# Kernel optimization log

Hardware: AMD Instinct MI355X
Metric: run time of the kernel (lower is better)

Reference implementation:

```python
import jax, jax.numpy as jnp
import numpy as np

EPS = 1e-7
B, C, IMG = 1024, 3, 32
NCLASS = 10
N_IN, L_IN, L_OUT = 64, 16, 16   # primary caps: 64 capsules of length 16; digit caps length 16
R_ITER = 3


def squash(c, axis):
    dot = jnp.sum(c * c, axis=axis, keepdims=True)
    return dot / (1.0 + dot) / jnp.sqrt(dot + EPS) * c


def conv2d(x, w, b, stride):
    y = jax.lax.conv_general_dilated(x, w, (stride, stride), 'VALID',
                                     dimension_numbers=('NCHW', 'OIHW', 'NCHW'))
    return y + b[None, :, None, None]


def setup_inputs() -> dict:
    key = jax.random.key(0)
    ks = jax.random.split(key, 16)
    inp = {
        'x': jax.random.uniform(ks[0], (B, C, IMG, IMG), dtype=jnp.float32),
        'y': jax.random.randint(ks[1], (B,), 0, NCLASS, dtype=jnp.int64),
        'conv1_w': 0.05 * jax.random.normal(ks[2], (128, C, 3, 3), jnp.float32),
        'conv1_b': jnp.zeros((128,), jnp.float32),
        'conv2_w': 0.05 * jax.random.normal(ks[3], (256, 128, 5, 5), jnp.float32),
        'conv2_b': jnp.zeros((256,), jnp.float32),
        'conv3_w': 0.05 * jax.random.normal(ks[4], (256, 256, 5, 5), jnp.float32),
        'conv3_b': jnp.zeros((256,), jnp.float32),
        'caps_w': 0.05 * jax.random.normal(ks[5], (N_IN, NCLASS, L_IN, L_OUT), jnp.float32),
        'caps_b': 0.05 * jax.random.normal(ks[6], (NCLASS, L_OUT), jnp.float32),
        'fc1_w': 0.05 * jax.random.normal(ks[7], (512, NCLASS * L_OUT), jnp.float32),
        'fc1_b': jnp.zeros((512,), jnp.float32),
        'fc2_w': 0.05 * jax.random.normal(ks[8], (1024, 512), jnp.float32),
        'fc2_b': jnp.zeros((1024,), jnp.float32),
        'fc3_w': 0.05 * jax.random.normal(ks[9], (IMG * IMG * C, 1024), jnp.float32),
        'fc3_b': jnp.zeros((IMG * IMG * C,), jnp.float32),
    }
    return inp


def reference(x, y, conv1_w, conv1_b, conv2_w, conv2_b, conv3_w, conv3_b,
              caps_w, caps_b, fc1_w, fc1_b, fc2_w, fc2_b, fc3_w, fc3_b):
    # CNN blocks
    h = jax.nn.relu(conv2d(x, conv1_w, conv1_b, 2))   # [B,128,15,15]
    h = jax.nn.relu(conv2d(h, conv2_w, conv2_b, 2))   # [B,256,6,6]
    h = jax.nn.relu(conv2d(h, conv3_w, conv3_b, 1))   # [B,256,2,2]

    # Primary capsules: [B,64,16], squashed along capsule-length axis
    prim = squash(h.reshape(h.shape[0], N_IN, L_IN), axis=-1)

    # u_hat[b,i,o,j] = sum_k W[i,o,k,j] * prim[b,i,k]  -> [B,64,10,16]
    u_hat = jnp.einsum('bik,iokj->bioj', prim, caps_w)
    u_hat_det = jax.lax.stop_gradient(u_hat)

    b_ij = jnp.zeros((h.shape[0], N_IN, NCLASS), dtype=u_hat.dtype)
    v = None
    for r in range(R_ITER):
        c_ij = jax.nn.softmax(b_ij, axis=2)           # over output capsules
        uh = u_hat if r == R_ITER - 1 else u_hat_det
        s = jnp.einsum('bio,bioj->boj', c_ij, uh) + caps_b   # [B,10,16]
        v = squash(s, axis=-1)
        if r < R_ITER - 1:
            agree = jnp.einsum('bioj,boj->bio', u_hat_det, jax.lax.stop_gradient(v))
            b_ij = b_ij + agree

    # capsule lengths: [B,10,1,1]
    v_lengths = jnp.sqrt(jnp.sum(v * v, axis=-1, keepdims=True) + EPS)[..., None]

    # reconstruction (mask by true label one-hot)
    one_hot = jax.nn.one_hot(y, NCLASS, dtype=v.dtype)       # [B,10]
    masked = (v * one_hot[:, :, None]).reshape(v.shape[0], NCLASS * L_OUT)
    h1 = jax.nn.relu(masked @ fc1_w.T + fc1_b)
    h2 = jax.nn.relu(h1 @ fc2_w.T + fc2_b)
    decoded = jax.nn.sigmoid(h2 @ fc3_w.T + fc3_b)           # [B,3072]
    return (v_lengths, decoded)
```

## Files before the change

### kernel.cpp

```cpp
#include <hip/hip_runtime.h>
#include <hip/hip_bf16.h>
#include <math.h>

#define EPSF 1e-7f

typedef __attribute__((ext_vector_type(8))) short bhalf8;
typedef __attribute__((ext_vector_type(4))) float floatx4;

__global__ __launch_bounds__(256) void conv1_kernel(
    const float* __restrict__ x, const float* __restrict__ w,
    const float* __restrict__ bias, __hip_bfloat16* __restrict__ out)
{
  __shared__ float wl[4096];
  __shared__ float bl[128];
  const int b0 = blockIdx.x * 2;
  const int t = threadIdx.x;
  for (int i = t; i < 4096; i += 256) {
    int oc = i >> 5, q = i & 31;
    wl[i] = (q < 27) ? w[oc*27 + q] : 0.f;
  }
  if (t < 128) bl[t] = bias[t];
  __syncthreads();
  if (t >= 225) return;
  const int py = t / 15, px = t % 15;
  float win[2][28];
  win[0][27] = 0.f; win[1][27] = 0.f;
#pragma unroll
  for (int im = 0; im < 2; ++im) {
    const float* xb = x + (size_t)(b0 + im) * 3072;
#pragma unroll
    for (int c = 0; c < 3; ++c)
#pragma unroll
      for (int ky = 0; ky < 3; ++ky)
#pragma unroll
        for (int kx = 0; kx < 3; ++kx)
          win[im][c*9 + ky*3 + kx] = xb[c*1024 + (py*2 + ky)*32 + (px*2 + kx)];
  }
#pragma unroll 1
  for (int oc0 = 0; oc0 < 128; oc0 += 32) {
    __hip_bfloat16 hv[2][32];
#pragma unroll
    for (int oc = 0; oc < 32; ++oc) {
      const float4* wp = (const float4*)&wl[(oc0 + oc) << 5];
      float a0 = bl[oc0 + oc], a1 = a0;
#pragma unroll
      for (int qq = 0; qq < 7; ++qq) {
        float4 wv = wp[qq];
        a0 = fmaf(win[0][qq*4+0], wv.x, a0); a1 = fmaf(win[1][qq*4+0], wv.x, a1);
        a0 = fmaf(win[0][qq*4+1], wv.y, a0); a1 = fmaf(win[1][qq*4+1], wv.y, a1);
        a0 = fmaf(win[0][qq*4+2], wv.z, a0); a1 = fmaf(win[1][qq*4+2], wv.z, a1);
        a0 = fmaf(win[0][qq*4+3], wv.w, a0); a1 = fmaf(win[1][qq*4+3], wv.w, a1);
      }
      hv[0][oc] = __float2bfloat16(fmaxf(a0, 0.f));
      hv[1][oc] = __float2bfloat16(fmaxf(a1, 0.f));
    }
#pragma unroll
    for (int qq = 0; qq < 4; ++qq) {
      int c16 = (oc0 >> 3) + qq;
#pragma unroll
      for (int im = 0; im < 2; ++im) {
        const uint4* src = (const uint4*)hv[im];
        *(uint4*)((char*)out + (size_t)(b0+im)*57600 + c16*3600 + t*16) = src[qq];
      }
    }
  }
}

__global__ __launch_bounds__(256) void prep_kernel(
    const float* __restrict__ conv2w, const float* __restrict__ conv3w,
    const float* __restrict__ capsw,  const float* __restrict__ fc1w,
    const float* __restrict__ fc2w,   const float* __restrict__ fc3w,
    __hip_bfloat16* __restrict__ wt2, __hip_bfloat16* __restrict__ wt3,
    __hip_bfloat16* __restrict__ cwt, float* __restrict__ fc1wt,
    __hip_bfloat16* __restrict__ wf2, __hip_bfloat16* __restrict__ wf3)
{
  const int t = threadIdx.x;
  int b = blockIdx.x;
  if (b < 12288) {
    int i = b*256 + t;
    wf3[i] = __float2bfloat16(fc3w[i]);
    return;
  }
  b -= 12288;
  if (b < 6400) {
    int i = b*256 + t;
    int s = i >> 14, r = i & 16383;
    int oc = r >> 6, kq = r & 63;
    int k = s*64 + kq;
    int tap = k >> 8, ic = k & 255;
    wt3[i] = __float2bfloat16(conv3w[(oc*256 + ic)*25 + tap]);
    return;
  }
  b -= 6400;
  if (b < 3200) {
    int i = b*256 + t;
    int s = i >> 13, r = i & 8191;
    int oc = r >> 5, kq = r & 31;
    int h = (s >= 50) ? 1 : 0;
    int r2 = s - h*50;
    int tap = r2 >> 1, q = r2 & 1;
    int ic = h*64 + q*32 + kq;
    wt2[i] = __float2bfloat16(conv2w[(oc*128 + ic)*25 + tap]);
    return;
  }
  b -= 3200;
  if (b < 2048) {
    int i = b*256 + t;
    wf2[i] = __float2bfloat16(fc2w[i]);
    return;
  }
  b -= 2048;
  if (b < 640) {
    int i2 = b*256 + t;
    int k = i2 & 15, j = (i2 >> 4) & 15, io = i2 >> 8;
    cwt[i2] = __float2bfloat16(capsw[(io*16 + k)*16 + j]);
    return;
  }
  b -= 640;
  {
    int i = b*256 + t;
    int j = i >> 9, n = i & 511;
    fc1wt[i] = fc1w[n*160 + j];
  }
}

__global__ __launch_bounds__(1024) void conv2_mfma_v2_kernel(
    const __hip_bfloat16* __restrict__ a,
    const __hip_bfloat16* __restrict__ wt,
    const float* __restrict__ bias,
    __hip_bfloat16* __restrict__ out,
    int img_base)
{
  __shared__ __align__(16) unsigned short Il[4*225*64];
  const int b0   = img_base + blockIdx.x * 4;
  const int t    = threadIdx.x;
  const int lane = t & 63;
  const int w    = t >> 6;
  const int wm   = w >> 3;
  const int wn   = w & 7;
  const int n    = lane & 15;
  const int g    = lane >> 4;

  const char* gB = (const char*)wt + (wn*32 + n)*64 + g*16;
  bhalf8 b00 = *(const bhalf8*)(gB);
  bhalf8 b01 = *(const bhalf8*)(gB + 1024);
  bhalf8 b10 = *(const bhalf8*)(gB + 16384);
  bhalf8 b11 = *(const bhalf8*)(gB + 16384 + 1024);

  int Abase[5], em[5];
#pragma unroll
  for (int mt = 0; mt < 5; ++mt) {
    int tile = wm*5 + mt;
    int m = tile*16 + n;
    if (m >= 144) m = 0;
    int img = m / 36, pos = m - img*36;
    int py = pos / 6, px = pos - py*6;
    int pixb = 30*py + 2*px;
    Abase[mt] = (img*225 + pixb) * 128;
    em[mt] = g + m;
  }

  floatx4 acc[5][2];
#pragma unroll
  for (int mt = 0; mt < 5; ++mt)
#pragma unroll
    for (int nt = 0; nt < 2; ++nt)
      acc[mt][nt] = (floatx4){0.f, 0.f, 0.f, 0.f};

  int s = 0;
#pragma unroll 1
  for (int h = 0; h < 2; ++h) {
    if (h) __syncthreads();
    for (int i = t; i < 7200; i += 1024) {
      int img = i / 1800;
      int r = i - img*1800;
      int p = r >> 3, c = r & 7;
      uint4 v = *(const uint4*)((const char*)a +
                (size_t)(b0+img)*57600 + (h*8 + c)*3600 + p*16);
      int px15 = p % 15, py15 = p / 15;
      int csw = (c + (px15 >> 1) + 6*(py15 >> 1) + ((img & 1) << 2)) & 7;
      *(uint4*)((char*)Il + (img*225 + p)*128 + csw*16) = v;
    }
    __syncthreads();

    int dpix = 0, kx = 0, ky = 0;
#pragma unroll 1
    for (int tap = 0; tap < 25; ++tap) {
      const int doff = dpix << 7;
      const int dsw  = (kx >> 1) + 6*(ky >> 1);
      int a0[5];
#pragma unroll
      for (int mt = 0; mt < 5; ++mt)
        a0[mt] = Abase[mt] + doff + (((em[mt] + dsw) & 7) << 4);

#pragma unroll
      for (int mt = 0; mt < 4; ++mt) {
        bhalf8 av = *(const bhalf8*)((const char*)Il + a0[mt]);
        acc[mt][0] = __builtin_amdgcn_mfma_f32_16x16x32_bf16(av, b00, acc[mt][0], 0, 0, 0);
        acc[mt][1] = __builtin_amdgcn_mfma_f32_16x16x32_bf16(av, b01, acc[mt][1], 0, 0, 0);
      }
      if (wm == 0) {
        bhalf8 av = *(const bhalf8*)((const char*)Il + a0[4]);
        acc[4][0] = __builtin_amdgcn_mfma_f32_16x16x32_bf16(av, b00, acc[4][0], 0, 0, 0);
        acc[4][1] = __builtin_amdgcn_mfma_f32_16x16x32_bf16(av, b01, acc[4][1], 0, 0, 0);
      }
      {
        const int spre = (s + 2 < 100) ? (s + 2) : 99;
        b00 = *(const bhalf8*)(gB + (size_t)spre*16384);
        b01 = *(const bhalf8*)(gB + (size_t)spre*16384 + 1024);
      }
#pragma unroll
      for (int mt = 0; mt < 4; ++mt) {
        bhalf8 av = *(const bhalf8*)((const char*)Il + (a0[mt] ^ 64));
        acc[mt][0] = __builtin_amdgcn_mfma_f32_16x16x32_bf16(av, b10, acc[mt][0], 0, 0, 0);
        acc[mt][1] = __builtin_amdgcn_mfma_f32_16x16x32_bf16(av, b11, acc[mt][1], 0, 0, 0);
      }
      if (wm == 0) {
        bhalf8 av = *(const bhalf8*)((const char*)Il + (a0[4] ^ 64));
        acc[4][0] = __builtin_amdgcn_mfma_f32_16x16x32_bf16(av, b10, acc[4][0], 0, 0, 0);
        acc[4][1] = __builtin_amdgcn_mfma_f32_16x16x32_bf16(av, b11, acc[4][1], 0, 0, 0);
      }
      {
        const int spre = (s + 3 < 100) ? (s + 3) : 99;
        b10 = *(const bhalf8*)(gB + (size_t)spre*16384);
        b11 = *(const bhalf8*)(gB + (size_t)spre*16384 + 1024);
      }
      s += 2;
      if (kx == 4) { kx = 0; ++ky; dpix += 11; } else { ++kx; ++dpix; }
    }
  }

  const float bv0 = bias[wn*32 + n];
  const float bv1 = bias[wn*32 + 16 + n];
#pragma unroll
  for (int mt = 0; mt < 5; ++mt) {
    if (mt < 4 || wm == 0) {
      int tile = wm*5 + mt;
#pragma unroll
      for (int r = 0; r < 4; ++r) {
        int m = tile*16 + g*4 + r;
        int img = m / 36, pos = m - img*36;
        size_t o = (((size_t)(b0+img)*36 + pos) << 8) + wn*32 + n;
        out[o]      = __float2bfloat16(fmaxf(acc[mt][0][r] + bv0, 0.f));
        out[o + 16] = __float2bfloat16(fmaxf(acc[mt][1][r] + bv1, 0.f));
      }
    }
  }
}

__global__ __launch_bounds__(512) void conv3_mfma_kernel(
    const __hip_bfloat16* __restrict__ a,
    const __hip_bfloat16* __restrict__ wt,
    float* __restrict__ pout)
{
  __shared__ __align__(16) unsigned short Il[16*1448];
  const int b0   = blockIdx.x * 16;
  const int kq   = blockIdx.y;
  const int t    = threadIdx.x;
  const int lane = t & 63;
  const int w    = t >> 6;
  const int n    = lane & 15;
  const int g    = lane >> 4;

  for (int i = t; i < 2304; i += 512) {
    int img = i / 144, r = i - img*144;
    int p = r >> 2, c = r & 3;
    uint4 v = *(const uint4*)((const char*)a +
              ((((size_t)(b0+img)*36 + p) << 9) + kq*64 + c*16));
    *(uint4*)((char*)Il + (img*1448 + p*40 + c*8)*2) = v;
  }

  const char* gB = (const char*)wt + (size_t)(w*32 + n)*128 +
                   (kq & 1)*64 + g*16;
  const int kqs = kq >> 1;
  bhalf8 b00, b01, b10, b11;
  b00 = *(const bhalf8*)(gB + (size_t)(0*4 + kqs)*32768);
  b01 = *(const bhalf8*)(gB + (size_t)(0*4 + kqs)*32768 + 2048);
  b10 = *(const bhalf8*)(gB + (size_t)(1*4 + kqs)*32768);
  b11 = *(const bhalf8*)(gB + (size_t)(1*4 + kqs)*32768 + 2048);

  const int d = n >> 2, pos = n & 3;
  const int pb = (pos >> 1)*6 + (pos & 1);
  int ab[4];
#pragma unroll
  for (int mt = 0; mt < 4; ++mt)
    ab[mt] = ((mt*4 + d)*1448 + pb*40 + g*8) * 2;

  floatx4 acc[4][2];
#pragma unroll
  for (int mt = 0; mt < 4; ++mt)
#pragma unroll
    for (int nt = 0; nt < 2; ++nt)
      acc[mt][nt] = (floatx4){0.f, 0.f, 0.f, 0.f};

  __syncthreads();

  int toff = 0, kx = 0;
#pragma unroll 1
  for (int tap = 0; tap < 24; tap += 2) {
#pragma unroll
    for (int mt = 0; mt < 4; ++mt) {
      bhalf8 av = *(const bhalf8*)((const char*)Il + ab[mt] + toff*80);
      acc[mt][0] = __builtin_amdgcn_mfma_f32_16x16x32_bf16(av, b00, acc[mt][0], 0, 0, 0);
      acc[mt][1] = __builtin_amdgcn_mfma_f32_16x16x32_bf16(av, b01, acc[mt][1], 0, 0, 0);
    }
    b00 = *(const bhalf8*)(gB + (size_t)((tap+2)*4 + kqs)*32768);
    b01 = *(const bhalf8*)(gB + (size_t)((tap+2)*4 + kqs)*32768 + 2048);
    if (++kx == 5) { kx = 0; toff += 2; } else ++toff;
#pragma unroll
    for (int mt = 0; mt < 4; ++mt) {
      bhalf8 av = *(const bhalf8*)((const char*)Il + ab[mt] + toff*80);
      acc[mt][0] = __builtin_amdgcn_mfma_f32_16x16x32_bf16(av, b10, acc[mt][0], 0, 0, 0);
      acc[mt][1] = __builtin_amdgcn_mfma_f32_16x16x32_bf16(av, b11, acc[mt][1], 0, 0, 0);
    }
    {
      const int tpre = (tap + 3 <= 24) ? (tap + 3) : 24;
      b10 = *(const bhalf8*)(gB + (size_t)(tpre*4 + kqs)*32768);
      b11 = *(const bhalf8*)(gB + (size_t)(tpre*4 + kqs)*32768 + 2048);
    }
    if (++kx == 5) { kx = 0; toff += 2; } else ++toff;
  }
#pragma unroll
  for (int mt = 0; mt < 4; ++mt) {
    bhalf8 av = *(const bhalf8*)((const char*)Il + ab[mt] + toff*80);
    acc[mt][0] = __builtin_amdgcn_mfma_f32_16x16x32_bf16(av, b00, acc[mt][0], 0, 0, 0);
    acc[mt][1] = __builtin_amdgcn_mfma_f32_16x16x32_bf16(av, b01, acc[mt][1], 0, 0, 0);
  }

  float* po = pout + (size_t)kq*1048576;
#pragma unroll
  for (int mt = 0; mt < 4; ++mt) {
#pragma unroll
    for (int r = 0; r < 4; ++r) {
      int m = mt*16 + g*4 + r;
      int img = m >> 2, p2 = m & 3;
#pragma unroll
      for (int nt = 0; nt < 2; ++nt)
        po[((size_t)(b0+img)*256 + w*32 + nt*16 + n)*4 + p2] = acc[mt][nt][r];
    }
  }
}

__global__ __launch_bounds__(256) void caps_kernel(
    const float* __restrict__ pout, const __hip_bfloat16* __restrict__ cwt,
    const float* __restrict__ cb, const float* __restrict__ c3b,
    const int* __restrict__ y,
    const float* __restrict__ fc1wt, const float* __restrict__ fc1b,
    float* __restrict__ vlen, __hip_bfloat16* __restrict__ h1f)
{
  __shared__ float prim[1024];
  __shared__ float uh[10240];
  __shared__ float bij[640];
  __shared__ float cij[640];
  __shared__ float vv[160];
  const int b = blockIdx.x, t = threadIdx.x;
  {
    const float* pp = pout + (size_t)b*1024 + t*4;
    float4 s4 = *(const float4*)pp;
#pragma unroll
    for (int q = 1; q < 8; ++q) {
      float4 v = *(const float4*)(pp + (size_t)q*1048576);
      s4.x += v.x; s4.y += v.y; s4.z += v.z; s4.w += v.w;
    }
    const float bv = c3b[t];
    float4 h = make_float4(fmaxf(s4.x + bv, 0.f), fmaxf(s4.y + bv, 0.f),
                           fmaxf(s4.z + bv, 0.f), fmaxf(s4.w + bv, 0.f));
    float dd = h.x*h.x + h.y*h.y + h.z*h.z + h.w*h.w;
    dd += __shfl_xor(dd, 1);
    dd += __shfl_xor(dd, 2);
    float sc = dd / (1.f + dd) / sqrtf(dd + EPSF);
    float4 o4 = make_float4(h.x*sc, h.y*sc, h.z*sc, h.w*sc);
    *(float4*)&prim[t*4] = o4;
  }
  for (int f = t; f < 640; f += 256) bij[f] = 0.f;
  __syncthreads();
  for (int f = t; f < 10240; f += 256) {
    const int i = f / 160;
    const uint4* wv = (const uint4*)(cwt + (size_t)f*16);
    uint4 wa = wv[0], wb = wv[1];
    unsigned uw[8] = {wa.x, wa.y, wa.z, wa.w, wb.x, wb.y, wb.z, wb.w};
    const float* pp = prim + i*16;
    float s = 0.f;
#pragma unroll
    for (int q = 0; q < 8; ++q) {
      float lo = __uint_as_float(uw[q] << 16);
      float hi = __uint_as_float(uw[q] & 0xffff0000u);
      s = fmaf(pp[2*q],   lo, s);
      s = fmaf(pp[2*q+1], hi, s);
    }
    uh[f] = s;
  }
  __syncthreads();
  for (int r = 0; r < 3; ++r) {
    if (t < 64) {
      float e[10];
      float mx = -1e30f;
#pragma unroll
      for (int o = 0; o < 10; ++o) { e[o] = bij[t*10 + o]; mx = fmaxf(mx, e[o]); }
      float sum = 0.f;
#pragma unroll
      for (int o = 0; o < 10; ++o) { e[o] = expf(e[o] - mx); sum += e[o]; }
      float inv = 1.f / sum;
#pragma unroll
      for (int o = 0; o < 10; ++o) cij[t*10 + o] = e[o] * inv;
    }
    __syncthreads();
    if (t < 160) {
      const int o = t >> 4;
      float s0 = cb[t], s1 = 0.f, s2 = 0.f, s3 = 0.f;
      for (int i = 0; i < 64; i += 4) {
        s0 = fmaf(cij[(i+0)*10 + o], uh[(i+0)*160 + t], s0);
        s1 = fmaf(cij[(i+1)*10 + o], uh[(i+1)*160 + t], s1);
        s2 = fmaf(cij[(i+2)*10 + o], uh[(i+2)*160 + t], s2);
        s3 = fmaf(cij[(i+3)*10 + o], uh[(i+3)*160 + t], s3);
      }
      float s = (s0 + s1) + (s2 + s3);
      float dd = s*s;
      dd += __shfl_xor(dd, 1); dd += __shfl_xor(dd, 2);
      dd += __shfl_xor(dd, 4); dd += __shfl_xor(dd, 8);
      float sc = dd / (1.f + dd) / sqrtf(dd + EPSF);
      vv[t] = s * sc;
      if (r == 2 && (t & 15) == 0)
        vlen[b*10 + o] = sqrtf(sc*sc*dd + EPSF);
    }
    __syncthreads();
    if (r < 2) {
      for (int f = t; f < 640; f += 256) {
        int i = f / 10, o = f % 10;
        const float* up = &uh[i*160 + o*16];
        const float* vp = &vv[o*16];
        float a = 0.f;
#pragma unroll
        for (int j = 0; j < 16; ++j) a = fmaf(up[j], vp[j], a);
        bij[f] += a;
      }
      __syncthreads();
    }
  }
  const int yb = y[b];
  const float* vy = &vv[yb*16];
  for (int nn = t; nn < 512; nn += 256) {
    float s = fc1b[nn];
#pragma unroll
    for (int k = 0; k < 16; ++k)
      s = fmaf(vy[k], fc1wt[(yb*16 + k)*512 + nn], s);
    h1f[b*512 + nn] = __float2bfloat16(fmaxf(s, 0.f));
  }
}

template<int ACT, int MT, int NT>
__global__ __launch_bounds__(256) void fc_mfma_kernel(
    const __hip_bfloat16* __restrict__ A,
    const __hip_bfloat16* __restrict__ W,
    const float* __restrict__ bias,
    void* __restrict__ outv, int M, int N, int K)
{
  const int t    = threadIdx.x;
  const int lane = t & 63;
  const int w    = t >> 6;
  const int wr   = w >> 1, wc = w & 1;
  const int n    = lane & 15, g = lane >> 4;
  const int m0   = blockIdx.x * (2*MT*16) + wr*(MT*16);
  const int n0   = blockIdx.y * (2*NT*16) + wc*(NT*16);
  const __hip_bfloat16* Ap = A + (size_t)(m0 + n)*K + g*8;
  const __hip_bfloat16* Wp = W + (size_t)(n0 + n)*K + g*8;
  const int steps = K >> 5;

  bhalf8 aa0[MT], aa1[MT], bb0[NT], bb1[NT];
#pragma unroll
  for (int mt = 0; mt < MT; ++mt) {
    aa0[mt] = *(const bhalf8*)(Ap + (size_t)mt*16*K);
    aa1[mt] = *(const bhalf8*)(Ap + (size_t)mt*16*K + 32);
  }
#pragma unroll
  for (int nt = 0; nt < NT; ++nt) {
    bb0[nt] = *(const bhalf8*)(Wp + (size_t)nt*16*K);
    bb1[nt] = *(const bhalf8*)(Wp + (size_t)nt*16*K + 32);
  }

  floatx4 acc[MT][NT];
#pragma unroll
  for (int mt = 0; mt < MT; ++mt)
#pragma unroll
    for (int nt = 0; nt < NT; ++nt)
      acc[mt][nt] = (floatx4){0.f, 0.f, 0.f, 0.f};

#pragma unroll 1
  for (int s = 0; s < steps; s += 2) {
#pragma unroll
    for (int mt = 0; mt < MT; ++mt)
#pragma unroll
      for (int nt = 0; nt < NT; ++nt)
        acc[mt][nt] = __builtin_amdgcn_mfma_f32_16x16x32_bf16(
            aa0[mt], bb0[nt], acc[mt][nt], 0, 0, 0);
    {
      const int spre = (s + 2 < steps) ? (s + 2) : s;
#pragma unroll
      for (int mt = 0; mt < MT; ++mt)
        aa0[mt] = *(const bhalf8*)(Ap + (size_t)mt*16*K + spre*32);
#pragma unroll
      for (int nt = 0; nt < NT; ++nt)
        bb0[nt] = *(const bhalf8*)(Wp + (size_t)nt*16*K + spre*32);
    }
#pragma unroll
    for (int mt = 0; mt < MT; ++mt)
#pragma unroll
      for (int nt = 0; nt < NT; ++nt)
        acc[mt][nt] = __builtin_amdgcn_mfma_f32_16x16x32_bf16(
            aa1[mt], bb1[nt], acc[mt][nt], 0, 0, 0);
    {
      const int spre = (s + 3 < steps) ? (s + 3) : (s + 1);
#pragma unroll
      for (int mt = 0; mt < MT; ++mt)
        aa1[mt] = *(const bhalf8*)(Ap + (size_t)mt*16*K + spre*32);
#pragma unroll
      for (int nt = 0; nt < NT; ++nt)
        bb1[nt] = *(const bhalf8*)(Wp + (size_t)nt*16*K + spre*32);
    }
  }

#pragma unroll
  for (int mt = 0; mt < MT; ++mt) {
#pragma unroll
    for (int r = 0; r < 4; ++r) {
      const int m = m0 + mt*16 + g*4 + r;
#pragma unroll
      for (int nt = 0; nt < NT; ++nt) {
        const int col = n0 + nt*16 + n;
        float v = acc[mt][nt][r] + bias[col];
        if (ACT == 0) {
          ((__hip_bfloat16*)outv)[(size_t)m*N + col] =
              __float2bfloat16(fmaxf(v, 0.f));
        } else {
          ((float*)outv)[(size_t)m*N + col] = 1.f / (1.f + expf(-v));
        }
      }
    }
  }
}

extern "C" void kernel_launch(void* const* d_in, const int* in_sizes, int n_in,
                              void* d_out, int out_size, void* d_ws, size_t ws_size,
                              hipStream_t stream) {
  const float* x       = (const float*)d_in[0];
  const int*   y       = (const int*)  d_in[1];
  const float* conv1_w = (const float*)d_in[2];
  const float* conv1_b = (const float*)d_in[3];
  const float* conv2_w = (const float*)d_in[4];
  const float* conv2_b = (const float*)d_in[5];
  const float* conv3_w = (const float*)d_in[6];
  const float* conv3_b = (const float*)d_in[7];
  const float* caps_w  = (const float*)d_in[8];
  const float* caps_b  = (const float*)d_in[9];
  const float* fc1_w   = (const float*)d_in[10];
  const float* fc1_b   = (const float*)d_in[11];
  const float* fc2_w   = (const float*)d_in[12];
  const float* fc2_b   = (const float*)d_in[13];
  const float* fc3_w   = (const float*)d_in[14];
  const float* fc3_b   = (const float*)d_in[15];
  float* out = (float*)d_out;
  float* ws  = (float*)d_ws;

  __hip_bfloat16* h1t   = (__hip_bfloat16*)ws;
  __hip_bfloat16* wt2   = (__hip_bfloat16*)(ws + 14745600);
  __hip_bfloat16* wt3   = (__hip_bfloat16*)(ws + 15155200);
  __hip_bfloat16* h2t   = (__hip_bfloat16*)(ws + 15974400);
  float*          pout  = ws + 20692992;
  __hip_bfloat16* h1f   = (__hip_bfloat16*)(ws + 29081600);
  __hip_bfloat16* h2f   = (__hip_bfloat16*)(ws + 29343744);
  __hip_bfloat16* wf2   = (__hip_bfloat16*)(ws + 29868032);
  __hip_bfloat16* wf3   = (__hip_bfloat16*)(ws + 30130176);
  __hip_bfloat16* cwt   = (__hip_bfloat16*)(ws + 31703040);
  float*          fc1wt = ws + 31784960;

  prep_kernel<<<dim3(24896), 256, 0, stream>>>(
      conv2_w, conv3_w, caps_w, fc1_w, fc2_w, fc3_w,
      wt2, wt3, cwt, fc1wt, wf2, wf3);
  conv1_kernel<<<dim3(512),        256, 0, stream>>>(x, conv1_w, conv1_b, h1t);
  conv2_mfma_v2_kernel<<<dim3(256), 1024, 0, stream>>>(h1t, wt2, conv2_b, h2t, 0);
  conv3_mfma_kernel<<<dim3(64, 8), 512, 0, stream>>>(h2t, wt3, pout);
  caps_kernel<<<dim3(1024),        256, 0, stream>>>(pout, cwt, caps_b, conv3_b,
                                                     y, fc1wt, fc1_b, out, h1f);
  fc_mfma_kernel<0,2,2><<<dim3(16, 16), 256, 0, stream>>>(
      h1f, wf2, fc2_b, h2f, 1024, 1024, 512);
  fc_mfma_kernel<1,2,2><<<dim3(16, 48), 256, 0, stream>>>(
      h2f, wf3, fc3_b, out + 10240, 1024, 3072, 1024);
}
```

Measured before the change: 340.0 us.

## Split conv2 across two kernel variants and coalesce conv weight prep via LDS transpose

The conv2/conv3 weight repacking in the prep kernel now loads each output channel's contiguous weights into shared memory and writes the transposed bf16 layout from there, replacing strided global gathers with coalesced reads. Conv2 is split: the original 4-image, 1024-thread kernel handles the first 512 images over 128 blocks. A new 2-image, 512-thread variant with a 64-wide N tile per wave handles the remaining 512 images over 256 blocks. This is meant to improve block count and occupancy balance for conv2, at the cost of an extra launch and a second code path with boundary-masked tiles.

Result: slower. 393.1 us (+15.6%).

```diff
diff --git a/kernel.cpp b/kernel.cpp
--- a/kernel.cpp
+++ b/kernel.cpp
@@ -74,6 +74,7 @@
     __hip_bfloat16* __restrict__ cwt, float* __restrict__ fc1wt,
     __hip_bfloat16* __restrict__ wf2, __hip_bfloat16* __restrict__ wf3)
 {
+  __shared__ float tl[6400];
   const int t = threadIdx.x;
   int b = blockIdx.x;
   if (b < 12288) {
@@ -82,28 +83,6 @@
     return;
   }
   b -= 12288;
-  if (b < 6400) {
-    int i = b*256 + t;
-    int s = i >> 14, r = i & 16383;
-    int oc = r >> 6, kq = r & 63;
-    int k = s*64 + kq;
-    int tap = k >> 8, ic = k & 255;
-    wt3[i] = __float2bfloat16(conv3w[(oc*256 + ic)*25 + tap]);
-    return;
-  }
-  b -= 6400;
-  if (b < 3200) {
-    int i = b*256 + t;
-    int s = i >> 13, r = i & 8191;
-    int oc = r >> 5, kq = r & 31;
-    int h = (s >= 50) ? 1 : 0;
-    int r2 = s - h*50;
-    int tap = r2 >> 1, q = r2 & 1;
-    int ic = h*64 + q*32 + kq;
-    wt2[i] = __float2bfloat16(conv2w[(oc*128 + ic)*25 + tap]);
-    return;
-  }
-  b -= 3200;
   if (b < 2048) {
     int i = b*256 + t;
     wf2[i] = __float2bfloat16(fc2w[i]);
@@ -117,10 +96,43 @@
     return;
   }
   b -= 640;
-  {
+  if (b < 320) {
     int i = b*256 + t;
     int j = i >> 9, n = i & 511;
     fc1wt[i] = fc1w[n*160 + j];
+    return;
+  }
+  b -= 320;
+  if (b < 256) {
+    const float* src = conv3w + (size_t)b*6400;
+    for (int i = t; i < 6400; i += 256) tl[i] = src[i];
+    __syncthreads();
+#pragma unroll 1
+    for (int q = 0; q < 25; ++q) {
+      int j = q*256 + t;
+      int s = j >> 6, kq = j & 63;
+      int tap = j >> 8, ic = j & 255;
+      wt3[(size_t)s*16384 + b*64 + kq] = __float2bfloat16(tl[ic*25 + tap]);
+    }
+    return;
+  }
+  b -= 256;
+  {
+    const float* src = conv2w + (size_t)b*3200;
+    for (int i = t; i < 3200; i += 256) tl[i] = src[i];
+    __syncthreads();
+#pragma unroll 1
+    for (int q = 0; q < 13; ++q) {
+      int j = q*256 + t;
+      if (j < 3200) {
+        int s = j >> 5, kq = j & 31;
+        int h = (s >= 50) ? 1 : 0;
+        int r2 = s - h*50;
+        int tap = r2 >> 1, qq = r2 & 1;
+        int ic = h*64 + qq*32 + kq;
+        wt2[(size_t)s*8192 + b*32 + kq] = __float2bfloat16(tl[ic*25 + tap]);
+      }
+    }
   }
 }
 
@@ -243,6 +255,143 @@
         size_t o = (((size_t)(b0+img)*36 + pos) << 8) + wn*32 + n;
         out[o]      = __float2bfloat16(fmaxf(acc[mt][0][r] + bv0, 0.f));
         out[o + 16] = __float2bfloat16(fmaxf(acc[mt][1][r] + bv1, 0.f));
+      }
+    }
+  }
+}
+
+__global__ __launch_bounds__(512) void conv2_mfma_v5_kernel(
+    const __hip_bfloat16* __restrict__ a,
+    const __hip_bfloat16* __restrict__ wt,
+    const float* __restrict__ bias,
+    __hip_bfloat16* __restrict__ out,
+    int img_base)
+{
+  __shared__ __align__(16) unsigned short Il[2*225*64];
+  const int b0   = img_base + blockIdx.x * 2;
+  const int t    = threadIdx.x;
+  const int lane = t & 63;
+  const int w    = t >> 6;
+  const int wm   = w >> 2;
+  const int wn   = w & 3;
+  const int n    = lane & 15;
+  const int g    = lane >> 4;
+
+  const char* gB = (const char*)wt + (wn*64 + n)*64 + g*16;
+  bhalf8 bs0[4], bs1[4];
+#pragma unroll
+  for (int nt = 0; nt < 4; ++nt) {
+    bs0[nt] = *(const bhalf8*)(gB + nt*1024);
+    bs1[nt] = *(const bhalf8*)(gB + 16384 + nt*1024);
+  }
+
+  const int tbase = wm*3;
+  int Abase[3], em[3];
+#pragma unroll
+  for (int mt = 0; mt < 3; ++mt) {
+    int tile = tbase + mt;
+    int m = tile*16 + n;
+    if (m >= 72) m = 0;
+    int img = m / 36, pos = m - img*36;
+    int py = pos / 6, px = pos - py*6;
+    int pixb = 30*py + 2*px;
+    Abase[mt] = (img*225 + pixb) * 128;
+    em[mt] = g + m;
+  }
+
+  floatx4 acc[3][4];
+#pragma unroll
+  for (int mt = 0; mt < 3; ++mt)
+#pragma unroll
+    for (int nt = 0; nt < 4; ++nt)
+      acc[mt][nt] = (floatx4){0.f, 0.f, 0.f, 0.f};
+
+  int s = 0;
+#pragma unroll 1
+  for (int h = 0; h < 2; ++h) {
+    if (h) __syncthreads();
+    for (int i = t; i < 3600; i += 512) {
+      int img = i / 1800;
+      int r = i - img*1800;
+      int p = r >> 3, c = r & 7;
+      uint4 v = *(const uint4*)((const char*)a +
+                (size_t)(b0+img)*57600 + (h*8 + c)*3600 + p*16);
+      int px15 = p % 15, py15 = p / 15;
+      int csw = (c + (px15 >> 1) + 6*(py15 >> 1) + (img << 2)) & 7;
+      *(uint4*)((char*)Il + (img*225 + p)*128 + csw*16) = v;
+    }
+    __syncthreads();
+
+    int dpix = 0, kx = 0, ky = 0;
+#pragma unroll 1
+    for (int tap = 0; tap < 25; ++tap) {
+      const int doff = dpix << 7;
+      const int dsw  = (kx >> 1) + 6*(ky >> 1);
+      int a0[3];
+#pragma unroll
+      for (int mt = 0; mt < 3; ++mt)
+        a0[mt] = Abase[mt] + doff + (((em[mt] + dsw) & 7) << 4);
+
+#pragma unroll
+      for (int mt = 0; mt < 2; ++mt) {
+        bhalf8 av = *(const bhalf8*)((const char*)Il + a0[mt]);
+#pragma unroll
+        for (int nt = 0; nt < 4; ++nt)
+          acc[mt][nt] = __builtin_amdgcn_mfma_f32_16x16x32_bf16(av, bs0[nt], acc[mt][nt], 0, 0, 0);
+      }
+      if (wm == 0) {
+        bhalf8 av = *(const bhalf8*)((const char*)Il + a0[2]);
+#pragma unroll
+        for (int nt = 0; nt < 4; ++nt)
+          acc[2][nt] = __builtin_amdgcn_mfma_f32_16x16x32_bf16(av, bs0[nt], acc[2][nt], 0, 0, 0);
+      }
+      {
+        const int spre = (s + 2 < 100) ? (s + 2) : 99;
+#pragma unroll
+        for (int nt = 0; nt < 4; ++nt)
+          bs0[nt] = *(const bhalf8*)(gB + (size_t)spre*16384 + nt*1024);
+      }
+#pragma unroll
+      for (int mt = 0; mt < 2; ++mt) {
+        bhalf8 av = *(const bhalf8*)((const char*)Il + (a0[mt] ^ 64));
+#pragma unroll
+        for (int nt = 0; nt < 4; ++nt)
+          acc[mt][nt] = __builtin_amdgcn_mfma_f32_16x16x32_bf16(av, bs1[nt], acc[mt][nt], 0, 0, 0);
+      }
+      if (wm == 0) {
+        bhalf8 av = *(const bhalf8*)((const char*)Il + (a0[2] ^ 64));
+#pragma unroll
+        for (int nt = 0; nt < 4; ++nt)
+          acc[2][nt] = __builtin_amdgcn_mfma_f32_16x16x32_bf16(av, bs1[nt], acc[2][nt], 0, 0, 0);
+      }
+      {
+        const int spre = (s + 3 < 100) ? (s + 3) : 99;
+#pragma unroll
+        for (int nt = 0; nt < 4; ++nt)
+          bs1[nt] = *(const bhalf8*)(gB + (size_t)spre*16384 + nt*1024);
+      }
+      s += 2;
+      if (kx == 4) { kx = 0; ++ky; dpix += 11; } else { ++kx; ++dpix; }
+    }
+  }
+
+  float bv[4];
+#pragma unroll
+  for (int nt = 0; nt < 4; ++nt) bv[nt] = bias[wn*64 + nt*16 + n];
+#pragma unroll
+  for (int mt = 0; mt < 3; ++mt) {
+    if (mt < 2 || wm == 0) {
+      int tile = tbase + mt;
+#pragma unroll
+      for (int r = 0; r < 4; ++r) {
+        int m = tile*16 + g*4 + r;
+        if (m < 72) {
+          int img = m / 36, pos = m - img*36;
+          size_t o = (((size_t)(b0+img)*36 + pos) << 8) + wn*64 + n;
+#pragma unroll
+          for (int nt = 0; nt < 4; ++nt)
+            out[o + nt*16] = __float2bfloat16(fmaxf(acc[mt][nt][r] + bv[nt], 0.f));
+        }
       }
     }
   }
@@ -573,11 +722,12 @@
   __hip_bfloat16* cwt   = (__hip_bfloat16*)(ws + 31703040);
   float*          fc1wt = ws + 31784960;
 
-  prep_kernel<<<dim3(24896), 256, 0, stream>>>(
+  prep_kernel<<<dim3(15808), 256, 0, stream>>>(
       conv2_w, conv3_w, caps_w, fc1_w, fc2_w, fc3_w,
       wt2, wt3, cwt, fc1wt, wf2, wf3);
   conv1_kernel<<<dim3(512),        256, 0, stream>>>(x, conv1_w, conv1_b, h1t);
-  conv2_mfma_v2_kernel<<<dim3(256), 1024, 0, stream>>>(h1t, wt2, conv2_b, h2t, 0);
+  conv2_mfma_v2_kernel<<<dim3(128), 1024, 0, stream>>>(h1t, wt2, conv2_b, h2t, 0);
+  conv2_mfma_v5_kernel<<<dim3(256),  512, 0, stream>>>(h1t, wt2, conv2_b, h2t, 512);
   conv3_mfma_kernel<<<dim3(64, 8), 512, 0, stream>>>(h2t, wt3, pout);
   caps_kernel<<<dim3(1024),        256, 0, stream>>>(pout, cwt, caps_b, conv3_b,
                                                      y, fc1wt, fc1_b, out, h1f);
```

## Fuse conv1 into weight-prep kernel and transpose conv weights via shared memory

Applied to the files above, without the earlier changes.

Merges the conv1 kernel into the weight preparation launch so both run concurrently in one grid, removing a launch and letting conv1 overlap with weight conversion. The conv2/conv3 weight reorders now stage each output channel's weights in shared memory before scattering, replacing strided global gathers with coalesced loads. The change adds shared memory use to every prep block, which may reduce occupancy for the simple conversion blocks.

Result: faster. 326.2 us (median of 2 runs) (-4.1%).

```diff
diff --git a/kernel.cpp b/kernel.cpp
--- a/kernel.cpp
+++ b/kernel.cpp
@@ -7,66 +7,9 @@
 typedef __attribute__((ext_vector_type(8))) short bhalf8;
 typedef __attribute__((ext_vector_type(4))) float floatx4;
 
-__global__ __launch_bounds__(256) void conv1_kernel(
-    const float* __restrict__ x, const float* __restrict__ w,
-    const float* __restrict__ bias, __hip_bfloat16* __restrict__ out)
-{
-  __shared__ float wl[4096];
-  __shared__ float bl[128];
-  const int b0 = blockIdx.x * 2;
-  const int t = threadIdx.x;
-  for (int i = t; i < 4096; i += 256) {
-    int oc = i >> 5, q = i & 31;
-    wl[i] = (q < 27) ? w[oc*27 + q] : 0.f;
-  }
-  if (t < 128) bl[t] = bias[t];
-  __syncthreads();
-  if (t >= 225) return;
-  const int py = t / 15, px = t % 15;
-  float win[2][28];
-  win[0][27] = 0.f; win[1][27] = 0.f;
-#pragma unroll
-  for (int im = 0; im < 2; ++im) {
-    const float* xb = x + (size_t)(b0 + im) * 3072;
-#pragma unroll
-    for (int c = 0; c < 3; ++c)
-#pragma unroll
-      for (int ky = 0; ky < 3; ++ky)
-#pragma unroll
-        for (int kx = 0; kx < 3; ++kx)
-          win[im][c*9 + ky*3 + kx] = xb[c*1024 + (py*2 + ky)*32 + (px*2 + kx)];
-  }
-#pragma unroll 1
-  for (int oc0 = 0; oc0 < 128; oc0 += 32) {
-    __hip_bfloat16 hv[2][32];
-#pragma unroll
-    for (int oc = 0; oc < 32; ++oc) {
-      const float4* wp = (const float4*)&wl[(oc0 + oc) << 5];
-      float a0 = bl[oc0 + oc], a1 = a0;
-#pragma unroll
-      for (int qq = 0; qq < 7; ++qq) {
-        float4 wv = wp[qq];
-        a0 = fmaf(win[0][qq*4+0], wv.x, a0); a1 = fmaf(win[1][qq*4+0], wv.x, a1);
-        a0 = fmaf(win[0][qq*4+1], wv.y, a0); a1 = fmaf(win[1][qq*4+1], wv.y, a1);
-        a0 = fmaf(win[0][qq*4+2], wv.z, a0); a1 = fmaf(win[1][qq*4+2], wv.z, a1);
-        a0 = fmaf(win[0][qq*4+3], wv.w, a0); a1 = fmaf(win[1][qq*4+3], wv.w, a1);
-      }
-      hv[0][oc] = __float2bfloat16(fmaxf(a0, 0.f));
-      hv[1][oc] = __float2bfloat16(fmaxf(a1, 0.f));
-    }
-#pragma unroll
-    for (int qq = 0; qq < 4; ++qq) {
-      int c16 = (oc0 >> 3) + qq;
-#pragma unroll
-      for (int im = 0; im < 2; ++im) {
-        const uint4* src = (const uint4*)hv[im];
-        *(uint4*)((char*)out + (size_t)(b0+im)*57600 + c16*3600 + t*16) = src[qq];
-      }
-    }
-  }
-}
-
-__global__ __launch_bounds__(256) void prep_kernel(
+__global__ __launch_bounds__(256) void prepc1_kernel(
+    const float* __restrict__ x,      const float* __restrict__ conv1w,
+    const float* __restrict__ conv1b, __hip_bfloat16* __restrict__ h1t,
     const float* __restrict__ conv2w, const float* __restrict__ conv3w,
     const float* __restrict__ capsw,  const float* __restrict__ fc1w,
     const float* __restrict__ fc2w,   const float* __restrict__ fc3w,
@@ -74,36 +17,72 @@
     __hip_bfloat16* __restrict__ cwt, float* __restrict__ fc1wt,
     __hip_bfloat16* __restrict__ wf2, __hip_bfloat16* __restrict__ wf3)
 {
+  __shared__ float sh[6400];
   const int t = threadIdx.x;
   int b = blockIdx.x;
+
+  if (b < 512) {
+    float* wl = sh;
+    float* bl = sh + 4096;
+    const int b0 = b * 2;
+    for (int i = t; i < 4096; i += 256) {
+      int oc = i >> 5, q = i & 31;
+      wl[i] = (q < 27) ? conv1w[oc*27 + q] : 0.f;
+    }
+    if (t < 128) bl[t] = conv1b[t];
+    __syncthreads();
+    if (t >= 225) return;
+    const int py = t / 15, px = t % 15;
+    float win[2][28];
+    win[0][27] = 0.f; win[1][27] = 0.f;
+#pragma unroll
+    for (int im = 0; im < 2; ++im) {
+      const float* xb = x + (size_t)(b0 + im) * 3072;
+#pragma unroll
+      for (int c = 0; c < 3; ++c)
+#pragma unroll
+        for (int ky = 0; ky < 3; ++ky)
+#pragma unroll
+          for (int kx = 0; kx < 3; ++kx)
+            win[im][c*9 + ky*3 + kx] = xb[c*1024 + (py*2 + ky)*32 + (px*2 + kx)];
+    }
+#pragma unroll 1
+    for (int oc0 = 0; oc0 < 128; oc0 += 32) {
+      __hip_bfloat16 hv[2][32];
+#pragma unroll
+      for (int oc = 0; oc < 32; ++oc) {
+        const float4* wp = (const float4*)&wl[(oc0 + oc) << 5];
+        float a0 = bl[oc0 + oc], a1 = a0;
+#pragma unroll
+        for (int qq = 0; qq < 7; ++qq) {
+          float4 wv = wp[qq];
+          a0 = fmaf(win[0][qq*4+0], wv.x, a0); a1 = fmaf(win[1][qq*4+0], wv.x, a1);
+          a0 = fmaf(win[0][qq*4+1], wv.y, a0); a1 = fmaf(win[1][qq*4+1], wv.y, a1);
+          a0 = fmaf(win[0][qq*4+2], wv.z, a0); a1 = fmaf(win[1][qq*4+2], wv.z, a1);
+          a0 = fmaf(win[0][qq*4+3], wv.w, a0); a1 = fmaf(win[1][qq*4+3], wv.w, a1);
+        }
+        hv[0][oc] = __float2bfloat16(fmaxf(a0, 0.f));
+        hv[1][oc] = __float2bfloat16(fmaxf(a1, 0.f));
+      }
+#pragma unroll
+      for (int qq = 0; qq < 4; ++qq) {
+        int c16 = (oc0 >> 3) + qq;
+#pragma unroll
+        for (int im = 0; im < 2; ++im) {
+          const uint4* src = (const uint4*)hv[im];
+          *(uint4*)((char*)h1t + (size_t)(b0+im)*57600 + c16*3600 + t*16) = src[qq];
+        }
+      }
+    }
+    return;
+  }
+  b -= 512;
   if (b < 12288) {
     int i = b*256 + t;
     wf3[i] = __float2bfloat16(fc3w[i]);
     return;
   }
   b -= 12288;
-  if (b < 6400) {
-    int i = b*256 + t;
-    int s = i >> 14, r = i & 16383;
-    int oc = r >> 6, kq = r & 63;
-    int k = s*64 + kq;
-    int tap = k >> 8, ic = k & 255;
-    wt3[i] = __float2bfloat16(conv3w[(oc*256 + ic)*25 + tap]);
-    return;
-  }
-  b -= 6400;
-  if (b < 3200) {
-    int i = b*256 + t;
-    int s = i >> 13, r = i & 8191;
-    int oc = r >> 5, kq = r & 31;
-    int h = (s >= 50) ? 1 : 0;
-    int r2 = s - h*50;
-    int tap = r2 >> 1, q = r2 & 1;
-    int ic = h*64 + q*32 + kq;
-    wt2[i] = __float2bfloat16(conv2w[(oc*128 + ic)*25 + tap]);
-    return;
-  }
-  b -= 3200;
   if (b < 2048) {
     int i = b*256 + t;
     wf2[i] = __float2bfloat16(fc2w[i]);
@@ -117,10 +96,45 @@
     return;
   }
   b -= 640;
-  {
+  if (b < 320) {
     int i = b*256 + t;
     int j = i >> 9, n = i & 511;
     fc1wt[i] = fc1w[n*160 + j];
+    return;
+  }
+  b -= 320;
+  if (b < 256) {
+    float* tl = sh;
+    const float* src = conv3w + (size_t)b*6400;
+    for (int i = t; i < 6400; i += 256) tl[i] = src[i];
+    __syncthreads();
+#pragma unroll 1
+    for (int q = 0; q < 25; ++q) {
+      int j = q*256 + t;
+      int s = j >> 6, kq = j & 63;
+      int tap = j >> 8, ic = j & 255;
+      wt3[(size_t)s*16384 + b*64 + kq] = __float2bfloat16(tl[ic*25 + tap]);
+    }
+    return;
+  }
+  b -= 256;
+  {
+    float* tl = sh;
+    const float* src = conv2w + (size_t)b*3200;
+    for (int i = t; i < 3200; i += 256) tl[i] = src[i];
+    __syncthreads();
+#pragma unroll 1
+    for (int q = 0; q < 13; ++q) {
+      int j = q*256 + t;
+      if (j < 3200) {
+        int s = j >> 5, kq = j & 31;
+        int h = (s >= 50) ? 1 : 0;
+        int r2 = s - h*50;
+        int tap = r2 >> 1, qq = r2 & 1;
+        int ic = h*64 + qq*32 + kq;
+        wt2[(size_t)s*8192 + b*32 + kq] = __float2bfloat16(tl[ic*25 + tap]);
+      }
+    }
   }
 }
 
@@ -573,10 +587,10 @@
   __hip_bfloat16* cwt   = (__hip_bfloat16*)(ws + 31703040);
   float*          fc1wt = ws + 31784960;
 
-  prep_kernel<<<dim3(24896), 256, 0, stream>>>(
+  prepc1_kernel<<<dim3(16320), 256, 0, stream>>>(
+      x, conv1_w, conv1_b, h1t,
       conv2_w, conv3_w, caps_w, fc1_w, fc2_w, fc3_w,
       wt2, wt3, cwt, fc1wt, wf2, wf3);
-  conv1_kernel<<<dim3(512),        256, 0, stream>>>(x, conv1_w, conv1_b, h1t);
   conv2_mfma_v2_kernel<<<dim3(256), 1024, 0, stream>>>(h1t, wt2, conv2_b, h2t, 0);
   conv3_mfma_kernel<<<dim3(64, 8), 512, 0, stream>>>(h2t, wt3, pout);
   caps_kernel<<<dim3(1024),        256, 0, stream>>>(pout, cwt, caps_b, conv3_b,
```
